# Kernel tuning notes

Measured on AMD Instinct MI355X. Metric: run time of the kernel, lower is better.

Reference implementation:

```python
import jax, jax.numpy as jnp
import numpy as np
from jax import lax

B, CIN, H, W = 2, 512, 64, 64
NCLS = 5
CI = CIN // 4      # inter_channels = 128
CQ = CI // 8       # PAM query/key channels = 16
EPS = 1e-5


def setup_inputs() -> dict:
    key = jax.random.key(0)
    it = iter(jax.random.split(key, 48))

    def nrm(shape, s=0.05):
        return jax.random.normal(next(it), shape, jnp.float32) * s

    def bn(c):
        w = jax.random.uniform(next(it), (c,), jnp.float32, 0.5, 1.5)
        b = nrm((c,))
        m = nrm((c,))
        v = jax.random.uniform(next(it), (c,), jnp.float32, 0.5, 1.5)
        return w, b, m, v

    inp = {}
    inp['x'] = jax.random.normal(next(it), (B, CIN, H, W), jnp.float32)
    inp['bn_a_w'], inp['bn_a_b'], inp['bn_a_m'], inp['bn_a_v'] = bn(CIN)
    inp['conv_a_w'] = nrm((CI, CIN, 3, 3))
    inp['bn_c_w'], inp['bn_c_b'], inp['bn_c_m'], inp['bn_c_v'] = bn(CIN)
    inp['conv_c_w'] = nrm((CI, CIN, 3, 3))
    inp['pam_q_w'] = nrm((CQ, CI)); inp['pam_q_b'] = nrm((CQ,))
    inp['pam_k_w'] = nrm((CQ, CI)); inp['pam_k_b'] = nrm((CQ,))
    inp['pam_v_w'] = nrm((CI, CI)); inp['pam_v_b'] = nrm((CI,))
    inp['pam_gamma'] = nrm((1,), 0.5)
    inp['cam_gamma'] = nrm((1,), 0.5)
    inp['bn_a1_w'], inp['bn_a1_b'], inp['bn_a1_m'], inp['bn_a1_v'] = bn(CI)
    inp['conv_a1_w'] = nrm((CIN, CI)); inp['conv_a1_b'] = nrm((CIN,))
    inp['bn_c1_w'], inp['bn_c1_b'], inp['bn_c1_m'], inp['bn_c1_v'] = bn(CI)
    inp['conv_c1_w'] = nrm((CIN, CI)); inp['conv_c1_b'] = nrm((CIN,))
    inp['out_a_w'] = nrm((NCLS, CIN)); inp['out_a_b'] = nrm((NCLS,))
    inp['out_c_w'] = nrm((NCLS, CIN)); inp['out_c_b'] = nrm((NCLS,))
    inp['out_f_w'] = nrm((NCLS, CIN)); inp['out_f_b'] = nrm((NCLS,))
    return inp


def _bn_relu(x, w, b, m, v):
    # eval-mode BatchNorm2d followed by ReLU
    scale = (w / jnp.sqrt(v + EPS))[None, :, None, None]
    shift = (b - m * w / jnp.sqrt(v + EPS))[None, :, None, None]
    return jax.nn.relu(x * scale + shift)


def _conv3(x, w):
    return lax.conv_general_dilated(x, w, (1, 1), 'SAME',
                                    dimension_numbers=('NCHW', 'OIHW', 'NCHW'))


def _conv1(x, w, b):
    # 1x1 conv as channel matmul
    return jnp.einsum('oi,bihw->bohw', w, x) + b[None, :, None, None]


def _pam(x, wq, bq, wk, bk, wv, bv, gamma):
    Bc, C, Hh, Ww = x.shape
    N = Hh * Ww
    q = _conv1(x, wq, bq).reshape(Bc, -1, N)   # [B,CQ,N]
    k = _conv1(x, wk, bk).reshape(Bc, -1, N)   # [B,CQ,N]
    v = _conv1(x, wv, bv).reshape(Bc, C, N)    # [B,C,N]
    energy = jnp.einsum('bcn,bcm->bnm', q, k)  # [B,N,N]
    attn = jax.nn.softmax(energy, axis=-1)
    out = jnp.einsum('bcm,bnm->bcn', v, attn).reshape(Bc, C, Hh, Ww)
    return gamma * out + x


def _cam(x, gamma):
    Bc, C, Hh, Ww = x.shape
    N = Hh * Ww
    f = x.reshape(Bc, C, N)
    energy = jnp.einsum('bcn,bdn->bcd', f, f)                    # [B,C,C]
    energy_new = jnp.max(energy, -1, keepdims=True) - energy
    attn = jax.nn.softmax(energy_new, axis=-1)
    out = jnp.einsum('bcd,bdn->bcn', attn, f).reshape(Bc, C, Hh, Ww)
    return gamma * out + x


def reference(x, bn_a_w, bn_a_b, bn_a_m, bn_a_v, conv_a_w,
              bn_c_w, bn_c_b, bn_c_m, bn_c_v, conv_c_w,
              pam_q_w, pam_q_b, pam_k_w, pam_k_b, pam_v_w, pam_v_b,
              pam_gamma, cam_gamma,
              bn_a1_w, bn_a1_b, bn_a1_m, bn_a1_v, conv_a1_w, conv_a1_b,
              bn_c1_w, bn_c1_b, bn_c1_m, bn_c1_v, conv_c1_w, conv_c1_b,
              out_a_w, out_a_b, out_c_w, out_c_b, out_f_w, out_f_b):
    # position-attention branch
    sa = _conv3(_bn_relu(x, bn_a_w, bn_a_b, bn_a_m, bn_a_v), conv_a_w)
    sa = _pam(sa, pam_q_w, pam_q_b, pam_k_w, pam_k_b, pam_v_w, pam_v_b, pam_gamma)
    sa = _conv1(_bn_relu(sa, bn_a1_w, bn_a1_b, bn_a1_m, bn_a1_v), conv_a1_w, conv_a1_b)
    # channel-attention branch
    sc = _conv3(_bn_relu(x, bn_c_w, bn_c_b, bn_c_m, bn_c_v), conv_c_w)
    sc = _cam(sc, cam_gamma)
    sc = _conv1(_bn_relu(sc, bn_c1_w, bn_c1_b, bn_c1_m, bn_c1_v), conv_c1_w, conv_c1_b)
    feat_fusion = sa + sc
    # dropout is identity at eval time
    sa_out = _conv1(sa, out_a_w, out_a_b)
    sc_out = _conv1(sc, out_c_w, out_c_b)
    sasc_out = _conv1(feat_fusion, out_f_w, out_f_b)
    return (feat_fusion, sasc_out, sa_out, sc_out)
```

## Files before the change

kernel.cpp:

```cpp
#include <hip/hip_runtime.h>

using u16 = unsigned short;
using short8 = __attribute__((ext_vector_type(8))) short;
using f32x4 = __attribute__((ext_vector_type(4))) float;

struct alignas(8) U16x4 { u16 x, y, z, w; };

__device__ __forceinline__ float bf2f(u16 u) {
  return __uint_as_float(((unsigned int)u) << 16);
}
__device__ __forceinline__ u16 f2bf(float f) {
  unsigned int u = __float_as_uint(f);
  unsigned int r = u + 0x7FFFu + ((u >> 16) & 1u);
  return (u16)(r >> 16);
}

__global__ void k_prep_w(const float* __restrict__ wa, const float* __restrict__ wc,
                         u16* __restrict__ Wb) {
  int idx = blockIdx.x * 256 + threadIdx.x;
  int j = idx & 7;
  int l = (idx >> 3) & 63;
  int ks = (idx >> 9) & 3;
  int rest = idx >> 11;
  int tap = rest % 9;
  int rest2 = rest / 9;
  int chunk = rest2 & 3;
  int mt = (rest2 >> 2) & 7;
  int br = rest2 >> 5;
  int co = mt * 16 + (l & 15);
  int ci = chunk * 128 + ks * 32 + (l >> 4) * 8 + j;
  const float* w = br ? wc : wa;
  Wb[idx] = f2bf(w[co * 4608 + ci * 9 + tap]);
}

__global__ void k_prep_w1(const float* __restrict__ wa, const float* __restrict__ wc,
                          u16* __restrict__ W1b) {
  int idx = blockIdx.x * 256 + threadIdx.x;
  int j = idx & 7;
  int l = (idx >> 3) & 63;
  int ks = (idx >> 9) & 3;
  int cot = (idx >> 11) & 31;
  int br = idx >> 16;
  int co = cot * 16 + (l & 15);
  int ci = ks * 32 + (l >> 4) * 8 + j;
  const float* w = br ? wc : wa;
  W1b[idx] = f2bf(w[co * 128 + ci]);
}

__global__ void k_prep_wqkv(const float* __restrict__ wq, const float* __restrict__ wk,
                            const float* __restrict__ wv, u16* __restrict__ Wq) {
  int idx = blockIdx.x * 256 + threadIdx.x;
  if (idx >= 20480) return;
  int j = idx & 7;
  int l = (idx >> 3) & 63;
  int ks = (idx >> 9) & 3;
  int cot = idx >> 11;
  int co = cot * 16 + (l & 15);
  int ci = ks * 32 + (l >> 4) * 8 + j;
  float w = co < 16 ? wq[co * 128 + ci]
          : (co < 32 ? wk[(co - 16) * 128 + ci] : wv[(co - 32) * 128 + ci]);
  Wq[idx] = f2bf(w);
}

__global__ __launch_bounds__(256) void k_bnrelu2t(const float* __restrict__ x,
    const float* __restrict__ wa, const float* __restrict__ ba,
    const float* __restrict__ ma, const float* __restrict__ va,
    const float* __restrict__ wc, const float* __restrict__ bc,
    const float* __restrict__ mc, const float* __restrict__ vc,
    u16* __restrict__ xa16, u16* __restrict__ xcb16) {
  __shared__ float sA[512], bA[512], sC[512], bC[512];
  __shared__ u16 ta[64 * 136], tc[64 * 136];
  int t = threadIdx.x;
  int h = blockIdx.x, b = blockIdx.y;
  for (int c = t; c < 512; c += 256) {
    float s1 = wa[c] * rsqrtf(va[c] + 1e-5f);
    sA[c] = s1; bA[c] = ba[c] - ma[c] * s1;
    float s2 = wc[c] * rsqrtf(vc[c] + 1e-5f);
    sC[c] = s2; bC[c] = bc[c] - mc[c] * s2;
  }
  __syncthreads();
  const float* xb = x + ((size_t)b << 21) + (h << 6);
  u16* oa = xa16 + ((size_t)b << 21) + ((size_t)h << 15);
  u16* oc = xcb16 + ((size_t)b << 21) + ((size_t)h << 15);
  int w = t & 63, cg = t >> 6;
  for (int c0 = 0; c0 < 512; c0 += 128) {
#pragma unroll
    for (int i = 0; i < 8; ++i) {
      int cl = cg * 4 + i * 16;
      int c = c0 + cl;
      const float* xp = xb + (size_t)c * 4096 + w;
      float v0 = xp[0], v1 = xp[4096], v2 = xp[8192], v3 = xp[12288];
      U16x4 pa, pc;
      pa.x = f2bf(fmaxf(fmaf(v0, sA[c], bA[c]), 0.f));
      pa.y = f2bf(fmaxf(fmaf(v1, sA[c + 1], bA[c + 1]), 0.f));
      pa.z = f2bf(fmaxf(fmaf(v2, sA[c + 2], bA[c + 2]), 0.f));
      pa.w = f2bf(fmaxf(fmaf(v3, sA[c + 3], bA[c + 3]), 0.f));
      pc.x = f2bf(fmaxf(fmaf(v0, sC[c], bC[c]), 0.f));
      pc.y = f2bf(fmaxf(fmaf(v1, sC[c + 1], bC[c + 1]), 0.f));
      pc.z = f2bf(fmaxf(fmaf(v2, sC[c + 2], bC[c + 2]), 0.f));
      pc.w = f2bf(fmaxf(fmaf(v3, sC[c + 3], bC[c + 3]), 0.f));
      *(U16x4*)(ta + w * 136 + cl) = pa;
      *(U16x4*)(tc + w * 136 + cl) = pc;
    }
    __syncthreads();
#pragma unroll
    for (int i = 0; i < 4; ++i) {
      int idx = t + i * 256;
      int ww = idx >> 4, c8 = (idx & 15) << 3;
      *(short8*)(oa + (size_t)ww * 512 + c0 + c8) = *(const short8*)(ta + ww * 136 + c8);
      *(short8*)(oc + (size_t)ww * 512 + c0 + c8) = *(const short8*)(tc + ww * 136 + c8);
    }
    __syncthreads();
  }
}

__global__ __launch_bounds__(256, 2) void k_conv3n(
    const u16* __restrict__ xa16, const u16* __restrict__ xcb16,
    const u16* __restrict__ Wb,
    float* __restrict__ sa0, float* __restrict__ sc0,
    u16* __restrict__ sa_nhwc, u16* __restrict__ sc16h, u16* __restrict__ sc16l) {
  __shared__ u16 xs[3 * 66 * 136];
  int t = threadIdx.x;
  int h = blockIdx.x;
  int z = blockIdx.y; int b = z & 1, br = z >> 1;
  int cosplit = blockIdx.z;
  const u16* xb = (br ? xcb16 : xa16) + ((size_t)b << 21);
  const u16* wb = Wb + (size_t)br * 589824;
  float* out = (br ? sc0 : sa0) + (((size_t)b * 128) << 12) + (h << 6);

  int lane = t & 63, wave = t >> 6;
  int mi = lane & 15, quad = lane >> 4;
  int mt = cosplit * 4 + wave;

  if (t < 96) {
    int dh = t >> 5, side = (t >> 4) & 1, c8 = t & 15;
    short8 z8 = {0, 0, 0, 0, 0, 0, 0, 0};
    *(short8*)(xs + (dh * 66 + side * 65) * 136 + c8 * 8) = z8;
  }

  f32x4 acc[4] = {};

  const u16* wlane = wb + lane * 8;
  const u16* bbase0 = xs + mi * 136 + quad * 8;

  for (int chunk = 0; chunk < 4; ++chunk) {
    int ci0 = chunk << 7;
    __syncthreads();
#pragma unroll
    for (int dh = 0; dh < 3; ++dh) {
      int hh = h + dh - 1;
      bool val = (hh >= 0) && (hh < 64);
      const u16* src = xb + (((size_t)hh << 6) << 9) + ci0;
#pragma unroll
      for (int i = 0; i < 4; ++i) {
        int idx = t + i * 256;
        int w = idx >> 4, c8 = (idx & 15) << 3;
        short8 v = {0, 0, 0, 0, 0, 0, 0, 0};
        if (val) v = *(const short8*)(src + ((size_t)w << 9) + c8);
        *(short8*)(xs + (dh * 66 + 1 + w) * 136 + c8) = v;
      }
    }
    __syncthreads();
    const u16* wchunk = wlane + (size_t)(mt * 4 + chunk) * 18432;
    short8 wreg[2][4];
#pragma unroll
    for (int ks = 0; ks < 4; ++ks)
      wreg[0][ks] = *(const short8*)(wchunk + ks * 512);
#pragma unroll
    for (int tap = 0; tap < 9; ++tap) {
      const int cb = tap & 1;
      if (tap < 8) {
        const u16* wn = wchunk + (tap + 1) * 2048;
#pragma unroll
        for (int ks = 0; ks < 4; ++ks)
          wreg[cb ^ 1][ks] = *(const short8*)(wn + ks * 512);
      }
      const int dh = tap / 3, dw = tap % 3;
      const u16* bp = bbase0 + (dh * 66 + dw) * 136;
#pragma unroll
      for (int ks = 0; ks < 4; ++ks) {
        short8 a = wreg[cb][ks];
#pragma unroll
        for (int nt = 0; nt < 4; ++nt) {
          short8 bf = *(const short8*)(bp + nt * 2176 + ks * 32);
          acc[nt] = __builtin_amdgcn_mfma_f32_16x16x32_bf16(a, bf, acc[nt], 0, 0, 0);
        }
      }
    }
  }
#pragma unroll
  for (int nt = 0; nt < 4; ++nt)
#pragma unroll
    for (int r = 0; r < 4; ++r) {
      int co = mt * 16 + quad * 4 + r;
      out[((size_t)co << 12) + nt * 16 + mi] = acc[nt][r];
    }
  if (br == 0) {
    u16* dstq = sa_nhwc + ((size_t)b << 19) + ((size_t)h << 6) * 128;
#pragma unroll
    for (int nt = 0; nt < 4; ++nt) {
      U16x4 v4;
      v4.x = f2bf(acc[nt][0]); v4.y = f2bf(acc[nt][1]);
      v4.z = f2bf(acc[nt][2]); v4.w = f2bf(acc[nt][3]);
      *(U16x4*)(dstq + (size_t)(nt * 16 + mi) * 128 + mt * 16 + quad * 4) = v4;
    }
  } else {
    u16* dh_ = sc16h + ((size_t)b << 19) + (h << 6);
    u16* dl_ = sc16l + ((size_t)b << 19) + (h << 6);
#pragma unroll
    for (int nt = 0; nt < 4; ++nt)
#pragma unroll
      for (int r = 0; r < 4; ++r) {
        int co = mt * 16 + quad * 4 + r;
        float xv = acc[nt][r];
        u16 hi = f2bf(xv);
        float lo = xv - bf2f(hi);
        size_t o = ((size_t)co << 12) + nt * 16 + mi;
        dh_[o] = hi;
        dl_[o] = f2bf(lo);
      }
  }
}

__global__ __launch_bounds__(256) void k_qkv(
    const u16* __restrict__ sa_nhwc, const u16* __restrict__ Wqkvb,
    const float* __restrict__ bq, const float* __restrict__ bk,
    const float* __restrict__ bv,
    float* __restrict__ qb, float* __restrict__ kbuf, u16* __restrict__ vt16) {
  __shared__ float bs[160];
  int t = threadIdx.x;
  int b = blockIdx.y, n0 = blockIdx.x * 128;
  if (t < 160) bs[t] = t < 16 ? bq[t] : (t < 32 ? bk[t - 16] : bv[t - 32]);
  __syncthreads();
  int lane = t & 63, wave = t >> 6;
  int mi = lane & 15, quad = lane >> 4;
  const u16* xb = sa_nhwc + ((size_t)b << 19) + (size_t)n0 * 128;
  const u16* wb = Wqkvb + lane * 8;
  f32x4 acc[2][10] = {};
  short8 bf[2][4];
#pragma unroll
  for (int ns = 0; ns < 2; ++ns) {
    int n = wave * 32 + ns * 16 + mi;
#pragma unroll
    for (int ks = 0; ks < 4; ++ks)
      bf[ns][ks] = *(const short8*)(xb + (size_t)n * 128 + ks * 32 + quad * 8);
  }
#pragma unroll
  for (int cot = 0; cot < 10; ++cot) {
    short8 a0 = *(const short8*)(wb + (size_t)(cot * 4 + 0) * 512);
    short8 a1 = *(const short8*)(wb + (size_t)(cot * 4 + 1) * 512);
    short8 a2 = *(const short8*)(wb + (size_t)(cot * 4 + 2) * 512);
    short8 a3 = *(const short8*)(wb + (size_t)(cot * 4 + 3) * 512);
#pragma unroll
    for (int ns = 0; ns < 2; ++ns) {
      acc[ns][cot] = __builtin_amdgcn_mfma_f32_16x16x32_bf16(a0, bf[ns][0], acc[ns][cot], 0, 0, 0);
      acc[ns][cot] = __builtin_amdgcn_mfma_f32_16x16x32_bf16(a1, bf[ns][1], acc[ns][cot], 0, 0, 0);
      acc[ns][cot] = __builtin_amdgcn_mfma_f32_16x16x32_bf16(a2, bf[ns][2], acc[ns][cot], 0, 0, 0);
      acc[ns][cot] = __builtin_amdgcn_mfma_f32_16x16x32_bf16(a3, bf[ns][3], acc[ns][cot], 0, 0, 0);
    }
  }
#pragma unroll
  for (int cot = 0; cot < 10; ++cot)
#pragma unroll
    for (int ns = 0; ns < 2; ++ns)
#pragma unroll
      for (int r = 0; r < 4; ++r) {
        int co = cot * 16 + quad * 4 + r;
        int n = n0 + wave * 32 + ns * 16 + mi;
        float v = acc[ns][cot][r] + bs[co];
        if (co < 16) qb[((b * 16 + co) << 12) + n] = v;
        else if (co < 32) kbuf[((b * 16 + co - 16) << 12) + n] = v;
        else vt16[((size_t)(b * 128 + co - 32) << 12) + n] = f2bf(v);
      }
}

__global__ __launch_bounds__(256) void k_pam_stats(const float* __restrict__ qb,
    const float* __restrict__ kb, float* __restrict__ rmax, float* __restrict__ rinv) {
  int t = threadIdx.x, lane = t & 63, wid = t >> 6;
  int b = blockIdx.y;
  int n0 = blockIdx.x * 16 + wid * 4;
  float qreg[4][16];
  const float* qp = qb + ((size_t)b * 16 << 12) + n0;
#pragma unroll
  for (int ch = 0; ch < 16; ++ch)
#pragma unroll
    for (int j = 0; j < 4; ++j) qreg[j][ch] = qp[(ch << 12) + j];
  const float* kp = kb + ((size_t)b * 16 << 12);
  float mx[4], se[4];
#pragma unroll
  for (int j = 0; j < 4; ++j) { mx[j] = -1e30f; se[j] = 0.f; }
  for (int m4 = lane * 4; m4 < 4096; m4 += 256) {
    float e[4][4] = {};
#pragma unroll
    for (int ch = 0; ch < 16; ++ch) {
      float4 kv = *(const float4*)(kp + (ch << 12) + m4);
#pragma unroll
      for (int j = 0; j < 4; ++j) {
        float qv = qreg[j][ch];
        e[j][0] = fmaf(qv, kv.x, e[j][0]);
        e[j][1] = fmaf(qv, kv.y, e[j][1]);
        e[j][2] = fmaf(qv, kv.z, e[j][2]);
        e[j][3] = fmaf(qv, kv.w, e[j][3]);
      }
    }
#pragma unroll
    for (int j = 0; j < 4; ++j) {
      float lm = fmaxf(fmaxf(e[j][0], e[j][1]), fmaxf(e[j][2], e[j][3]));
      float nm = fmaxf(mx[j], lm);
      se[j] = se[j] * __expf(mx[j] - nm)
            + __expf(e[j][0] - nm) + __expf(e[j][1] - nm)
            + __expf(e[j][2] - nm) + __expf(e[j][3] - nm);
      mx[j] = nm;
    }
  }
#pragma unroll
  for (int off = 32; off >= 1; off >>= 1) {
#pragma unroll
    for (int j = 0; j < 4; ++j) {
      float om = __shfl_xor(mx[j], off);
      float os = __shfl_xor(se[j], off);
      float nm = fmaxf(mx[j], om);
      se[j] = se[j] * __expf(mx[j] - nm) + os * __expf(om - nm);
      mx[j] = nm;
    }
  }
  if (lane == 0) {
#pragma unroll
    for (int j = 0; j < 4; ++j) {
      rmax[(b << 12) + n0 + j] = mx[j];
      rinv[(b << 12) + n0 + j] = 1.f / se[j];
    }
  }
}

__global__ __launch_bounds__(512, 4) void k_pam_pv(const float* __restrict__ qb,
    const float* __restrict__ kb, const u16* __restrict__ vt16,
    const float* __restrict__ rmax, const float* __restrict__ rinv,
    const float* __restrict__ gamma, float* __restrict__ pvpart) {
  constexpr int PSTR = 264;
  __shared__ float ks[2][16 * 256];
  __shared__ u16 pL[32 * PSTR];
  int t = threadIdx.x;
  int b = blockIdx.y, n0 = blockIdx.x * 32;
  int mbeg = blockIdx.z << 11;
  int lane = t & 63, wave = t >> 6;
  int nl = t & 31, mg = t >> 5;
  int mi = lane & 15, quad = lane >> 4;
  int c0 = wave * 16;
  float qreg[16];
  const float* qp = qb + ((size_t)b * 16 << 12) + n0 + nl;
#pragma unroll
  for (int ch = 0; ch < 16; ++ch) qreg[ch] = qp[ch << 12];
  float mv = rmax[(b << 12) + n0 + nl];
  float iv = rinv[(b << 12) + n0 + nl];
  const float* kpb = kb + ((size_t)b * 16 << 12) + mbeg;
  const u16* vb = vt16 + ((size_t)b * 128 << 12);
  f32x4 acc[2] = {};
#pragma unroll
  for (int k = 0; k < 8; ++k) {
    int idx = t + k * 512;
    ks[0][idx] = kpb[((idx >> 8) << 12) + (idx & 255)];
  }
  __syncthreads();
  int cur = 0;
  for (int it = 0; it < 8; ++it) {
    int m0 = mbeg + (it << 8);
    short8 vreg[8];
#pragma unroll
    for (int ksl = 0; ksl < 8; ++ksl)
      vreg[ksl] = *(const short8*)(vb + ((size_t)(c0 + mi) << 12) + m0 + ksl * 32 + quad * 8);
    float kreg[8];
    if (it < 7) {
#pragma unroll
      for (int k = 0; k < 8; ++k) {
        int idx = t + k * 512;
        kreg[k] = kpb[((idx >> 8) << 12) + ((it + 1) << 8) + (idx & 255)];
      }
    }
    float e[16] = {};
    const float* kbase = &ks[cur][mg << 4];
#pragma unroll
    for (int ch = 0; ch < 16; ++ch) {
      float qv = qreg[ch];
      const float* kp2 = kbase + (ch << 8);
      float4 kv0 = *(const float4*)(kp2);
      float4 kv1 = *(const float4*)(kp2 + 4);
      float4 kv2 = *(const float4*)(kp2 + 8);
      float4 kv3 = *(const float4*)(kp2 + 12);
      e[0] = fmaf(qv, kv0.x, e[0]);  e[1] = fmaf(qv, kv0.y, e[1]);
      e[2] = fmaf(qv, kv0.z, e[2]);  e[3] = fmaf(qv, kv0.w, e[3]);
      e[4] = fmaf(qv, kv1.x, e[4]);  e[5] = fmaf(qv, kv1.y, e[5]);
      e[6] = fmaf(qv, kv1.z, e[6]);  e[7] = fmaf(qv, kv1.w, e[7]);
      e[8] = fmaf(qv, kv2.x, e[8]);  e[9] = fmaf(qv, kv2.y, e[9]);
      e[10] = fmaf(qv, kv2.z, e[10]); e[11] = fmaf(qv, kv2.w, e[11]);
      e[12] = fmaf(qv, kv3.x, e[12]); e[13] = fmaf(qv, kv3.y, e[13]);
      e[14] = fmaf(qv, kv3.z, e[14]); e[15] = fmaf(qv, kv3.w, e[15]);
    }
    short8 p0, p1;
#pragma unroll
    for (int j = 0; j < 8; ++j) {
      p0[j] = (short)f2bf(__expf(fminf(e[j] - mv, 0.f)) * iv);
      p1[j] = (short)f2bf(__expf(fminf(e[j + 8] - mv, 0.f)) * iv);
    }
    {
      u16* pw = pL + nl * PSTR + (mg << 4);
      *(short8*)(pw) = p0;
      *(short8*)(pw + 8) = p1;
    }
    __syncthreads();
    if (it < 7) {
#pragma unroll
      for (int k = 0; k < 8; ++k) {
        int idx = t + k * 512;
        ks[cur ^ 1][idx] = kreg[k];
      }
    }
#pragma unroll
    for (int ksl = 0; ksl < 8; ++ksl) {
      const u16* pb0 = pL + mi * PSTR + ksl * 32 + quad * 8;
      short8 b0 = *(const short8*)(pb0);
      short8 b1 = *(const short8*)(pb0 + 16 * PSTR);
      acc[0] = __builtin_amdgcn_mfma_f32_16x16x32_bf16(vreg[ksl], b0, acc[0], 0, 0, 0);
      acc[1] = __builtin_amdgcn_mfma_f32_16x16x32_bf16(vreg[ksl], b1, acc[1], 0, 0, 0);
    }
    __syncthreads();
    cur ^= 1;
  }
  float g = gamma[0];
  float* dst = pvpart + (((size_t)(blockIdx.z * 2 + b) * 128) << 12);
#pragma unroll
  for (int nh = 0; nh < 2; ++nh)
#pragma unroll
    for (int r = 0; r < 4; ++r) {
      int c = c0 + quad * 4 + r;
      dst[((size_t)c << 12) + n0 + nh * 16 + mi] = g * acc[nh][r];
    }
}

__global__ __launch_bounds__(512) void k_cam_energy_m(
    const u16* __restrict__ sc16h, const u16* __restrict__ sc16l,
    float* __restrict__ epart) {
  int t = threadIdx.x;
  int ti = blockIdx.x, kc = blockIdx.y, b = blockIdx.z;
  int lane = t & 63, wave = t >> 6;
  int mi = lane & 15, quad = lane >> 4;
  const u16* fh = sc16h + ((size_t)b << 19);
  const u16* fl = sc16l + ((size_t)b << 19);
  size_t ao = ((size_t)(ti * 16 + mi) << 12) + (kc << 9) + quad * 8;
  size_t bo = ((size_t)(wave * 16 + mi) << 12) + (kc << 9) + quad * 8;
  const u16* ah = fh + ao; const u16* al = fl + ao;
  const u16* bh = fh + bo; const u16* bl = fl + bo;
  f32x4 acc = {};
#pragma unroll
  for (int k = 0; k < 16; ++k) {
    short8 vah = *(const short8*)(ah + k * 32);
    short8 val = *(const short8*)(al + k * 32);
    short8 vbh = *(const short8*)(bh + k * 32);
    short8 vbl = *(const short8*)(bl + k * 32);
    acc = __builtin_amdgcn_mfma_f32_16x16x32_bf16(vah, vbh, acc, 0, 0, 0);
    acc = __builtin_amdgcn_mfma_f32_16x16x32_bf16(vah, vbl, acc, 0, 0, 0);
    acc = __builtin_amdgcn_mfma_f32_16x16x32_bf16(val, vbh, acc, 0, 0, 0);
  }
  float* ep = epart + (((size_t)(kc * 2 + b)) << 14);
#pragma unroll
  for (int r = 0; r < 4; ++r)
    ep[((ti * 16 + quad * 4 + r) << 7) + wave * 16 + mi] = acc[r];
}

__global__ void k_cam_softmax(const float* __restrict__ epart, float* __restrict__ attn) {
  int lane = threadIdx.x;
  int c = blockIdx.x, b = blockIdx.y;
  float e0 = 0.f, e1 = 0.f;
#pragma unroll
  for (int kc = 0; kc < 8; ++kc) {
    const float* ep = epart + (((size_t)(kc * 2 + b)) << 14) + (c << 7);
    e0 += ep[lane];
    e1 += ep[lane + 64];
  }
  float mn = fminf(e0, e1);
#pragma unroll
  for (int off = 32; off >= 1; off >>= 1) mn = fminf(mn, __shfl_xor(mn, off));
  float p0 = __expf(fminf(mn - e0, 0.f)), p1 = __expf(fminf(mn - e1, 0.f));
  float s = p0 + p1;
#pragma unroll
  for (int off = 32; off >= 1; off >>= 1) s += __shfl_xor(s, off);
  float inv = 1.f / s;
  float* a = attn + ((b * 128 + c) << 7);
  a[lane] = p0 * inv;
  a[lane + 64] = p1 * inv;
}

__global__ __launch_bounds__(256) void k_cam_out(const float* __restrict__ f,
    const float* __restrict__ attn, const float* __restrict__ gamma,
    float* __restrict__ sc1) {
  __shared__ float at2[128 * 16];
  int t = threadIdx.x;
  int b = blockIdx.z, c0 = blockIdx.y * 16;
  int n = blockIdx.x * 256 + t;
  for (int idx = t; idx < 2048; idx += 256) {
    int d = idx >> 4, cc = idx & 15;
    at2[idx] = attn[((b * 128 + c0 + cc) << 7) + d];
  }
  __syncthreads();
  float acc[16] = {};
  const float* fb = f + ((size_t)b * 128 << 12) + n;
  for (int d = 0; d < 128; ++d) {
    float fv = fb[d << 12];
    const float* ap = at2 + d * 16;
#pragma unroll
    for (int cc = 0; cc < 16; ++cc) acc[cc] = fmaf(ap[cc], fv, acc[cc]);
  }
  float g = gamma[0];
#pragma unroll
  for (int cc = 0; cc < 16; ++cc) {
    size_t o = ((size_t)(b * 128 + c0 + cc) << 12) + n;
    sc1[o] = fmaf(g, acc[cc], f[o]);
  }
}

__global__ __launch_bounds__(256, 2) void k_bout_m(
    const float* __restrict__ sa0, const float* __restrict__ pvpart,
    const float* __restrict__ sc1,
    const float* __restrict__ wa_, const float* __restrict__ ba_,
    const float* __restrict__ ma_, const float* __restrict__ va_,
    const float* __restrict__ wc_, const float* __restrict__ bc_,
    const float* __restrict__ mc_, const float* __restrict__ vc_,
    const u16* __restrict__ W1b, const float* __restrict__ Ba,
    const float* __restrict__ Bc,
    u16* __restrict__ sa2, u16* __restrict__ sc2) {
  __shared__ u16 xl[32 * 136];
  __shared__ float scl[128], shf[128];
  int t = threadIdx.x;
  int n0 = blockIdx.x * 32;
  int b = blockIdx.y, br = blockIdx.z;
  const float* bw = br ? wc_ : wa_;
  const float* bb = br ? bc_ : ba_;
  const float* bm = br ? mc_ : ma_;
  const float* bvv = br ? vc_ : va_;
  if (t < 128) {
    float s = bw[t] * rsqrtf(bvv[t] + 1e-5f);
    scl[t] = s;
    shf[t] = bb[t] - bm[t] * s;
  }
  __syncthreads();
  {
    int nl = t & 31, cio = t >> 5;
    const float* s0 = (br ? sc1 : sa0) + ((size_t)b * 128 << 12) + n0 + nl;
    const float* p0 = pvpart + ((size_t)b * 128 << 12) + n0 + nl;
    const float* p1 = pvpart + (((size_t)(2 + b) * 128) << 12) + n0 + nl;
#pragma unroll
    for (int half = 0; half < 2; ++half) {
      short8 v;
#pragma unroll
      for (int i = 0; i < 8; ++i) {
        int ci = cio * 16 + half * 8 + i;
        float xv = s0[(size_t)ci << 12];
        if (!br) xv += p0[(size_t)ci << 12] + p1[(size_t)ci << 12];
        v[i] = (short)f2bf(fmaxf(fmaf(xv, scl[ci], shf[ci]), 0.f));
      }
      *(short8*)(xl + nl * 136 + cio * 16 + half * 8) = v;
    }
  }
  __syncthreads();
  int lane = t & 63, wave = t >> 6;
  int mi = lane & 15, quad = lane >> 4;
  const u16* wb = W1b + (size_t)br * 65536 + lane * 8;
  f32x4 acc[8][2] = {};
#pragma unroll
  for (int ks = 0; ks < 4; ++ks) {
    short8 b0 = *(const short8*)(xl + mi * 136 + ks * 32 + quad * 8);
    short8 b1 = *(const short8*)(xl + (16 + mi) * 136 + ks * 32 + quad * 8);
#pragma unroll
    for (int ct = 0; ct < 8; ++ct) {
      int cot = wave * 8 + ct;
      short8 a = *(const short8*)(wb + ((size_t)(cot * 4 + ks) << 9));
      acc[ct][0] = __builtin_amdgcn_mfma_f32_16x16x32_bf16(a, b0, acc[ct][0], 0, 0, 0);
      acc[ct][1] = __builtin_amdgcn_mfma_f32_16x16x32_bf16(a, b1, acc[ct][1], 0, 0, 0);
    }
  }
  const float* Bs = br ? Bc : Ba;
  u16* dst = br ? sc2 : sa2;
#pragma unroll
  for (int ct = 0; ct < 8; ++ct)
#pragma unroll
    for (int nh = 0; nh < 2; ++nh)
#pragma unroll
      for (int r = 0; r < 4; ++r) {
        int co = (wave * 8 + ct) * 16 + quad * 4 + r;
        dst[((size_t)(b * 512 + co) << 12) + n0 + nh * 16 + mi] =
            f2bf(acc[ct][nh][r] + Bs[co]);
      }
}

__global__ __launch_bounds__(256) void k_heads(const u16* __restrict__ sa2,
    const u16* __restrict__ sc2,
    const float* __restrict__ wf, const float* __restrict__ wa, const float* __restrict__ wc,
    float* __restrict__ outFusion, float* __restrict__ clsacc) {
  __shared__ float lw[3 * 5 * 64];
  int t = threadIdx.x;
  int b = blockIdx.y, co0 = blockIdx.z * 64;
  int n = blockIdx.x * 256 + t;
  for (int idx = t; idx < 960; idx += 256) {
    int arr = idx / 320, rest = idx - arr * 320;
    int cls = rest >> 6, cc = rest & 63;
    const float* w = arr == 0 ? wf : (arr == 1 ? wa : wc);
    lw[idx] = w[cls * 512 + co0 + cc];
  }
  __syncthreads();
  float af[5] = {}, aa[5] = {}, ac[5] = {};
  for (int cc = 0; cc < 64; ++cc) {
    size_t o = ((size_t)(b * 512 + co0 + cc) << 12) + n;
    float a = bf2f(sa2[o]), c = bf2f(sc2[o]);
    float s = a + c;
    outFusion[o] = s;
#pragma unroll
    for (int cls = 0; cls < 5; ++cls) {
      af[cls] = fmaf(lw[0 * 320 + cls * 64 + cc], s, af[cls]);
      aa[cls] = fmaf(lw[1 * 320 + cls * 64 + cc], a, aa[cls]);
      ac[cls] = fmaf(lw[2 * 320 + cls * 64 + cc], c, ac[cls]);
    }
  }
#pragma unroll
  for (int cls = 0; cls < 5; ++cls) {
    int o = ((b * 5 + cls) << 12) + n;
    atomicAdd(&clsacc[o], af[cls]);
    atomicAdd(&clsacc[40960 + o], aa[cls]);
    atomicAdd(&clsacc[81920 + o], ac[cls]);
  }
}

__global__ void k_heads_final(const float* __restrict__ clsacc,
    const float* __restrict__ bf_, const float* __restrict__ ba_,
    const float* __restrict__ bc_, float* __restrict__ outCls) {
  int idx = blockIdx.x * 256 + threadIdx.x;
  int arr = idx / 40960;
  int rest = idx - arr * 40960;
  int cls = (rest >> 12) % 5;
  const float* bp = arr == 0 ? bf_ : (arr == 1 ? ba_ : bc_);
  outCls[idx] = clsacc[idx] + bp[cls];
}

extern "C" void kernel_launch(void* const* d_in, const int* in_sizes, int n_in,
                              void* d_out, int out_size, void* d_ws, size_t ws_size,
                              hipStream_t stream) {
  (void)in_sizes; (void)n_in; (void)out_size; (void)ws_size;
  const float* x      = (const float*)d_in[0];
  const float* bnaw   = (const float*)d_in[1];
  const float* bnab   = (const float*)d_in[2];
  const float* bnam   = (const float*)d_in[3];
  const float* bnav   = (const float*)d_in[4];
  const float* convaw = (const float*)d_in[5];
  const float* bncw   = (const float*)d_in[6];
  const float* bncb   = (const float*)d_in[7];
  const float* bncm   = (const float*)d_in[8];
  const float* bncv   = (const float*)d_in[9];
  const float* convcw = (const float*)d_in[10];
  const float* pqw    = (const float*)d_in[11];
  const float* pqb    = (const float*)d_in[12];
  const float* pkw    = (const float*)d_in[13];
  const float* pkb    = (const float*)d_in[14];
  const float* pvw    = (const float*)d_in[15];
  const float* pvb    = (const float*)d_in[16];
  const float* pgam   = (const float*)d_in[17];
  const float* cgam   = (const float*)d_in[18];
  const float* bna1w  = (const float*)d_in[19];
  const float* bna1b  = (const float*)d_in[20];
  const float* bna1m  = (const float*)d_in[21];
  const float* bna1v  = (const float*)d_in[22];
  const float* conva1w = (const float*)d_in[23];
  const float* conva1b = (const float*)d_in[24];
  const float* bnc1w  = (const float*)d_in[25];
  const float* bnc1b  = (const float*)d_in[26];
  const float* bnc1m  = (const float*)d_in[27];
  const float* bnc1v  = (const float*)d_in[28];
  const float* convc1w = (const float*)d_in[29];
  const float* convc1b = (const float*)d_in[30];
  const float* outaw  = (const float*)d_in[31];
  const float* outab  = (const float*)d_in[32];
  const float* outcw  = (const float*)d_in[33];
  const float* outcb  = (const float*)d_in[34];
  const float* outfw  = (const float*)d_in[35];
  const float* outfb  = (const float*)d_in[36];

  char* wsb = (char*)d_ws;
  size_t off = 0;
  auto take = [&](size_t bytes) -> void* {
    void* p = wsb + off;
    off += (bytes + 255) & ~(size_t)255;
    return p;
  };
  u16*   Wb    = (u16*)take((size_t)2 * 128 * 9 * 512 * 2);
  u16*   W1b   = (u16*)take((size_t)2 * 512 * 128 * 2);
  u16*   Wqkvb = (u16*)take((size_t)160 * 128 * 2);
  u16*   xa16  = (u16*)take((size_t)2 * 512 * 4096 * 2);
  u16*   xcb16 = (u16*)take((size_t)2 * 512 * 4096 * 2);
  float* sa0   = (float*)take((size_t)2 * 128 * 4096 * 4);
  float* sc0   = (float*)take((size_t)2 * 128 * 4096 * 4);
  u16*   sa_nhwc = (u16*)take((size_t)2 * 4096 * 128 * 2);
  u16*   sc16h = (u16*)take((size_t)2 * 128 * 4096 * 2);
  u16*   sc16l = (u16*)take((size_t)2 * 128 * 4096 * 2);
  float* qb    = (float*)take((size_t)2 * 16 * 4096 * 4);
  float* kbuf  = (float*)take((size_t)2 * 16 * 4096 * 4);
  u16*   vt16  = (u16*)take((size_t)2 * 128 * 4096 * 2);
  float* rmax  = (float*)take((size_t)2 * 4096 * 4);
  float* rinv  = (float*)take((size_t)2 * 4096 * 4);
  float* pvpart = (float*)take((size_t)2 * 2 * 128 * 4096 * 4);
  float* sc1   = (float*)take((size_t)2 * 128 * 4096 * 4);
  float* epart = (float*)take((size_t)8 * 2 * 128 * 128 * 4);
  float* attn  = (float*)take((size_t)2 * 128 * 128 * 4);
  u16*   sa2   = (u16*)take((size_t)2 * 512 * 4096 * 2);
  u16*   sc2   = (u16*)take((size_t)2 * 512 * 4096 * 2);
  float* clsacc = (float*)take((size_t)3 * 2 * 5 * 4096 * 4);

  float* outF = (float*)d_out;
  float* outCls = outF + (size_t)2 * 512 * 4096;

  hipMemsetAsync(clsacc, 0, (size_t)3 * 2 * 5 * 4096 * 4, stream);

  k_prep_w<<<4608, 256, 0, stream>>>(convaw, convcw, Wb);
  k_prep_w1<<<512, 256, 0, stream>>>(conva1w, convc1w, W1b);
  k_prep_wqkv<<<80, 256, 0, stream>>>(pqw, pkw, pvw, Wqkvb);
  k_bnrelu2t<<<dim3(64, 2), 256, 0, stream>>>(x, bnaw, bnab, bnam, bnav,
                                              bncw, bncb, bncm, bncv, xa16, xcb16);
  k_conv3n<<<dim3(64, 4, 2), 256, 0, stream>>>(xa16, xcb16, Wb, sa0, sc0,
                                               sa_nhwc, sc16h, sc16l);
  k_qkv<<<dim3(32, 2), 256, 0, stream>>>(sa_nhwc, Wqkvb, pqb, pkb, pvb,
                                         qb, kbuf, vt16);
  k_pam_stats<<<dim3(256, 2), 256, 0, stream>>>(qb, kbuf, rmax, rinv);
  k_pam_pv<<<dim3(128, 2, 2), 512, 0, stream>>>(qb, kbuf, vt16, rmax, rinv, pgam, pvpart);
  k_cam_energy_m<<<dim3(8, 8, 2), 512, 0, stream>>>(sc16h, sc16l, epart);
  k_cam_softmax<<<dim3(128, 2), 64, 0, stream>>>(epart, attn);
  k_cam_out<<<dim3(16, 8, 2), 256, 0, stream>>>(sc0, attn, cgam, sc1);
  k_bout_m<<<dim3(128, 2, 2), 256, 0, stream>>>(sa0, pvpart, sc1,
      bna1w, bna1b, bna1m, bna1v, bnc1w, bnc1b, bnc1m, bnc1v,
      W1b, conva1b, convc1b, sa2, sc2);
  k_heads<<<dim3(16, 2, 8), 256, 0, stream>>>(sa2, sc2, outfw, outaw, outcw, outF, clsacc);
  k_heads_final<<<480, 256, 0, stream>>>(clsacc, outfb, outab, outcb, outCls);
}
```

Measured before the change: 347.1 us.

## Compute PAM attention energies with split-bf16 MFMA instead of scalar FMAs

The q·k energy computation in the PAM P·V kernel moves from per-thread scalar fp32 FMA loops to bf16 MFMA instructions. Q and K are each split into a high and a low bf16 part to keep near-fp32 accuracy. K is restaged in LDS as bf16 hi/lo pairs in an m-major layout, and the exponentials are written to the P tile in the MFMA output layout. This cuts VALU work and LDS bandwidth for the score step, at the cost of extra conversion work when staging K and a small loss of precision from dropping the lo·lo term.

```diff
diff --git a/kernel.cpp b/kernel.cpp
--- a/kernel.cpp
+++ b/kernel.cpp
@@ -337,31 +337,47 @@
     const float* __restrict__ kb, const u16* __restrict__ vt16,
     const float* __restrict__ rmax, const float* __restrict__ rinv,
     const float* __restrict__ gamma, float* __restrict__ pvpart) {
+  constexpr int KSTR = 40;
   constexpr int PSTR = 264;
-  __shared__ float ks[2][16 * 256];
+  __shared__ u16 kst[2][256 * KSTR];
   __shared__ u16 pL[32 * PSTR];
+  __shared__ u16 qfh[32 * 16], qfl[32 * 16];
   int t = threadIdx.x;
   int b = blockIdx.y, n0 = blockIdx.x * 32;
   int mbeg = blockIdx.z << 11;
   int lane = t & 63, wave = t >> 6;
-  int nl = t & 31, mg = t >> 5;
   int mi = lane & 15, quad = lane >> 4;
   int c0 = wave * 16;
-  float qreg[16];
-  const float* qp = qb + ((size_t)b * 16 << 12) + n0 + nl;
-#pragma unroll
-  for (int ch = 0; ch < 16; ++ch) qreg[ch] = qp[ch << 12];
-  float mv = rmax[(b << 12) + n0 + nl];
-  float iv = rinv[(b << 12) + n0 + nl];
+  {
+    int ch = t & 15, nl = t >> 4;
+    float qv = qb[((size_t)(b * 16 + ch) << 12) + n0 + nl];
+    u16 hi = f2bf(qv);
+    qfh[nl * 16 + ch] = hi;
+    qfl[nl * 16 + ch] = f2bf(qv - bf2f(hi));
+  }
+  float mv0 = rmax[(b << 12) + n0 + mi],      iv0 = rinv[(b << 12) + n0 + mi];
+  float mv1 = rmax[(b << 12) + n0 + 16 + mi], iv1 = rinv[(b << 12) + n0 + 16 + mi];
   const float* kpb = kb + ((size_t)b * 16 << 12) + mbeg;
   const u16* vb = vt16 + ((size_t)b * 128 << 12);
   f32x4 acc[2] = {};
-#pragma unroll
-  for (int k = 0; k < 8; ++k) {
-    int idx = t + k * 512;
-    ks[0][idx] = kpb[((idx >> 8) << 12) + (idx & 255)];
+  int sm = t & 255, sc = t >> 8;
+  {
+    u16* kw = kst[0] + sm * KSTR + sc;
+#pragma unroll
+    for (int k = 0; k < 8; ++k) {
+      float v = kpb[((size_t)(sc + 2 * k) << 12) + sm];
+      u16 hi = f2bf(v);
+      kw[2 * k] = hi;
+      kw[16 + 2 * k] = f2bf(v - bf2f(hi));
+    }
   }
   __syncthreads();
+  int qoff = (quad & 1) * 8;
+  short8 bq1[2], bq2[2];
+  bq1[0] = *(const short8*)(qfh + mi * 16 + qoff);
+  bq1[1] = *(const short8*)(qfh + (16 + mi) * 16 + qoff);
+  bq2[0] = *(const short8*)(qfl + mi * 16 + qoff);
+  bq2[1] = *(const short8*)(qfl + (16 + mi) * 16 + qoff);
   int cur = 0;
   for (int it = 0; it < 8; ++it) {
     int m0 = mbeg + (it << 8);
@@ -372,47 +388,54 @@
     float kreg[8];
     if (it < 7) {
 #pragma unroll
-      for (int k = 0; k < 8; ++k) {
-        int idx = t + k * 512;
-        kreg[k] = kpb[((idx >> 8) << 12) + ((it + 1) << 8) + (idx & 255)];
-      }
-    }
-    float e[16] = {};
-    const float* kbase = &ks[cur][mg << 4];
-#pragma unroll
-    for (int ch = 0; ch < 16; ++ch) {
-      float qv = qreg[ch];
-      const float* kp2 = kbase + (ch << 8);
-      float4 kv0 = *(const float4*)(kp2);
-      float4 kv1 = *(const float4*)(kp2 + 4);
-      float4 kv2 = *(const float4*)(kp2 + 8);
-      float4 kv3 = *(const float4*)(kp2 + 12);
-      e[0] = fmaf(qv, kv0.x, e[0]);  e[1] = fmaf(qv, kv0.y, e[1]);
-      e[2] = fmaf(qv, kv0.z, e[2]);  e[3] = fmaf(qv, kv0.w, e[3]);
-      e[4] = fmaf(qv, kv1.x, e[4]);  e[5] = fmaf(qv, kv1.y, e[5]);
-      e[6] = fmaf(qv, kv1.z, e[6]);  e[7] = fmaf(qv, kv1.w, e[7]);
-      e[8] = fmaf(qv, kv2.x, e[8]);  e[9] = fmaf(qv, kv2.y, e[9]);
-      e[10] = fmaf(qv, kv2.z, e[10]); e[11] = fmaf(qv, kv2.w, e[11]);
-      e[12] = fmaf(qv, kv3.x, e[12]); e[13] = fmaf(qv, kv3.y, e[13]);
-      e[14] = fmaf(qv, kv3.z, e[14]); e[15] = fmaf(qv, kv3.w, e[15]);
-    }
-    short8 p0, p1;
-#pragma unroll
-    for (int j = 0; j < 8; ++j) {
-      p0[j] = (short)f2bf(__expf(fminf(e[j] - mv, 0.f)) * iv);
-      p1[j] = (short)f2bf(__expf(fminf(e[j + 8] - mv, 0.f)) * iv);
+      for (int k = 0; k < 8; ++k)
+        kreg[k] = kpb[((size_t)(sc + 2 * k) << 12) + ((it + 1) << 8) + sm];
     }
     {
-      u16* pw = pL + nl * PSTR + (mg << 4);
-      *(short8*)(pw) = p0;
-      *(short8*)(pw + 8) = p1;
+      const u16* ka = kst[cur] + (wave * 32) * KSTR;
+      short8 a0 = *(const short8*)(ka + mi * KSTR + quad * 8);
+      short8 a1 = *(const short8*)(ka + (16 + mi) * KSTR + quad * 8);
+      f32x4 e00 = {}, e01 = {}, e10 = {}, e11 = {};
+      e00 = __builtin_amdgcn_mfma_f32_16x16x32_bf16(a0, bq1[0], e00, 0, 0, 0);
+      e00 = __builtin_amdgcn_mfma_f32_16x16x32_bf16(a0, bq2[0], e00, 0, 0, 0);
+      e01 = __builtin_amdgcn_mfma_f32_16x16x32_bf16(a0, bq1[1], e01, 0, 0, 0);
+      e01 = __builtin_amdgcn_mfma_f32_16x16x32_bf16(a0, bq2[1], e01, 0, 0, 0);
+      e10 = __builtin_amdgcn_mfma_f32_16x16x32_bf16(a1, bq1[0], e10, 0, 0, 0);
+      e10 = __builtin_amdgcn_mfma_f32_16x16x32_bf16(a1, bq2[0], e10, 0, 0, 0);
+      e11 = __builtin_amdgcn_mfma_f32_16x16x32_bf16(a1, bq1[1], e11, 0, 0, 0);
+      e11 = __builtin_amdgcn_mfma_f32_16x16x32_bf16(a1, bq2[1], e11, 0, 0, 0);
+      u16* prow0 = pL + mi * PSTR + wave * 32 + quad * 4;
+      u16* prow1 = pL + (16 + mi) * PSTR + wave * 32 + quad * 4;
+      U16x4 p;
+      p.x = f2bf(__expf(fminf(e00[0] - mv0, 0.f)) * iv0);
+      p.y = f2bf(__expf(fminf(e00[1] - mv0, 0.f)) * iv0);
+      p.z = f2bf(__expf(fminf(e00[2] - mv0, 0.f)) * iv0);
+      p.w = f2bf(__expf(fminf(e00[3] - mv0, 0.f)) * iv0);
+      *(U16x4*)(prow0) = p;
+      p.x = f2bf(__expf(fminf(e10[0] - mv0, 0.f)) * iv0);
+      p.y = f2bf(__expf(fminf(e10[1] - mv0, 0.f)) * iv0);
+      p.z = f2bf(__expf(fminf(e10[2] - mv0, 0.f)) * iv0);
+      p.w = f2bf(__expf(fminf(e10[3] - mv0, 0.f)) * iv0);
+      *(U16x4*)(prow0 + 16) = p;
+      p.x = f2bf(__expf(fminf(e01[0] - mv1, 0.f)) * iv1);
+      p.y = f2bf(__expf(fminf(e01[1] - mv1, 0.f)) * iv1);
+      p.z = f2bf(__expf(fminf(e01[2] - mv1, 0.f)) * iv1);
+      p.w = f2bf(__expf(fminf(e01[3] - mv1, 0.f)) * iv1);
+      *(U16x4*)(prow1) = p;
+      p.x = f2bf(__expf(fminf(e11[0] - mv1, 0.f)) * iv1);
+      p.y = f2bf(__expf(fminf(e11[1] - mv1, 0.f)) * iv1);
+      p.z = f2bf(__expf(fminf(e11[2] - mv1, 0.f)) * iv1);
+      p.w = f2bf(__expf(fminf(e11[3] - mv1, 0.f)) * iv1);
+      *(U16x4*)(prow1 + 16) = p;
     }
     __syncthreads();
     if (it < 7) {
+      u16* kw = kst[cur ^ 1] + sm * KSTR + sc;
 #pragma unroll
       for (int k = 0; k < 8; ++k) {
-        int idx = t + k * 512;
-        ks[cur ^ 1][idx] = kreg[k];
+        u16 hi = f2bf(kreg[k]);
+        kw[2 * k] = hi;
+        kw[16 + 2 * k] = f2bf(kreg[k] - bf2f(hi));
       }
     }
 #pragma unroll
```

After: 341.6 us. Within noise of the previous version (-1.6%).
